# Optimization experiments

Hardware: AMD Instinct MI355X
Metric: run time of the kernel (lower is better)

Reference implementation:

```python
import jax, jax.numpy as jnp
import numpy as np

B, H, W, CP, CI = 2, 256, 256, 256, 256
IN, OUT = CP + CI, CP          # in_dims=512, out_dims=256
WS, NH, L = 8, 8, 2            # window, heads, num blocks
N = WS * WS                    # tokens per window
HD = OUT // NH                 # head dim = 32
SCALE = HD ** -0.5

def _rel_pos_index():
    c = np.stack(np.meshgrid(np.arange(WS), np.arange(WS), indexing='ij')).reshape(2, -1)
    r = (c[:, :, None] - c[:, None, :]).transpose(1, 2, 0)
    r[..., 0] += WS - 1
    r[..., 1] += WS - 1
    r[..., 0] *= 2 * WS - 1
    return r.sum(-1)  # [N, N] int

REL_IDX = _rel_pos_index()

def _attn_mask(shift):
    img = np.zeros((H, W))
    cnt = 0
    for hs in (slice(0, -WS), slice(-WS, -shift), slice(-shift, None)):
        for ws_ in (slice(0, -WS), slice(-WS, -shift), slice(-shift, None)):
            img[hs, ws_] = cnt
            cnt += 1
    m = img.reshape(H // WS, WS, W // WS, WS).transpose(0, 2, 1, 3).reshape(-1, N)
    d = m[:, None, :] - m[:, :, None]
    return jnp.asarray(np.where(d != 0, -100.0, 0.0).astype(np.float32))  # [nW, N, N]

MASK = _attn_mask(WS // 2)

def _ln(x, g, b, eps=1e-5):
    m = x.mean(-1, keepdims=True)
    v = ((x - m) ** 2).mean(-1, keepdims=True)
    return (x - m) * jax.lax.rsqrt(v + eps) * g + b

def _win_attn(x, qkv_w, qkv_b, rpb_t, proj_w, proj_b, shift):
    # x: [B,H,W,C]
    if shift > 0:
        x = jnp.roll(x, (-shift, -shift), axis=(1, 2))
    nW = (H // WS) * (W // WS)
    xw = x.reshape(B, H // WS, WS, W // WS, WS, OUT).transpose(0, 1, 3, 2, 4, 5).reshape(B, nW, N, OUT)
    qkv = (xw @ qkv_w.T + qkv_b).reshape(B, nW, N, 3, NH, HD)
    q, k, v = qkv[..., 0, :, :], qkv[..., 1, :, :], qkv[..., 2, :, :]  # [B,nW,N,NH,HD]
    attn = jnp.einsum('bwqhd,bwkhd->bwhqk', q * SCALE, k)  # [B,nW,NH,N,N]
    bias = rpb_t[REL_IDX.reshape(-1)].reshape(N, N, NH).transpose(2, 0, 1)  # [NH,N,N]
    attn = attn + bias
    if shift > 0:
        attn = attn + MASK[None, :, None, :, :]
    attn = jax.nn.softmax(attn, axis=-1)
    out = jnp.einsum('bwhqk,bwkhd->bwqhd', attn, v).reshape(B, nW, N, OUT)
    out = out @ proj_w.T + proj_b
    out = out.reshape(B, H // WS, W // WS, WS, WS, OUT).transpose(0, 1, 3, 2, 4, 5).reshape(B, H, W, OUT)
    if shift > 0:
        out = jnp.roll(out, (shift, shift), axis=(1, 2))
    return out

def setup_inputs() -> dict:
    key = jax.random.key(0)
    ks = jax.random.split(key, 12)
    s = 0.02
    p = {}
    p['pcd'] = jax.random.normal(ks[0], (B, H, W, CP), jnp.float32)
    p['img'] = jax.random.normal(ks[1], (B, H, W, CI), jnp.float32)
    p['rd_w1'] = jax.random.normal(ks[2], (4 * IN, IN), jnp.float32) * s
    p['rd_b1'] = jnp.zeros((4 * IN,), jnp.float32)
    p['rd_lng'] = jnp.ones((4 * IN,), jnp.float32)
    p['rd_lnb'] = jnp.zeros((4 * IN,), jnp.float32)
    p['rd_w2'] = jax.random.normal(ks[3], (OUT, 4 * IN), jnp.float32) * s
    p['rd_b2'] = jnp.zeros((OUT,), jnp.float32)
    p['n1g'] = jnp.ones((L, OUT), jnp.float32)
    p['n1b'] = jnp.zeros((L, OUT), jnp.float32)
    p['qkv_w'] = jax.random.normal(ks[4], (L, 3 * OUT, OUT), jnp.float32) * s
    p['qkv_b'] = jnp.zeros((L, 3 * OUT), jnp.float32)
    p['rpb'] = jax.random.normal(ks[5], (L, (2 * WS - 1) ** 2, NH), jnp.float32) * s
    p['proj_w'] = jax.random.normal(ks[6], (L, OUT, OUT), jnp.float32) * s
    p['proj_b'] = jnp.zeros((L, OUT), jnp.float32)
    p['n2g'] = jnp.ones((L, OUT), jnp.float32)
    p['n2b'] = jnp.zeros((L, OUT), jnp.float32)
    p['mlp_w1'] = jax.random.normal(ks[7], (L, 4 * OUT, OUT), jnp.float32) * s
    p['mlp_b1'] = jnp.zeros((L, 4 * OUT), jnp.float32)
    p['mlp_w2'] = jax.random.normal(ks[8], (L, OUT, 4 * OUT), jnp.float32) * s
    p['mlp_b2'] = jnp.zeros((L, OUT), jnp.float32)
    return p

def reference(pcd, img, rd_w1, rd_b1, rd_lng, rd_lnb, rd_w2, rd_b2,
              n1g, n1b, qkv_w, qkv_b, rpb, proj_w, proj_b,
              n2g, n2b, mlp_w1, mlp_b1, mlp_w2, mlp_b2):
    # reduce_dim: Linear -> LeakyReLU(0.01) -> LayerNorm -> Linear
    x = jnp.concatenate([pcd, img], axis=3)
    x = x @ rd_w1.T + rd_b1
    x = jnp.where(x > 0, x, 0.01 * x)
    x = _ln(x, rd_lng, rd_lnb)
    x = x @ rd_w2.T + rd_b2
    # two SwinTransformerBlocks (shift 0, then WS//2)
    for i in range(L):
        shift = 0 if i % 2 == 0 else WS // 2
        x = x + _win_attn(_ln(x, n1g[i], n1b[i]), qkv_w[i], qkv_b[i], rpb[i], proj_w[i], proj_b[i], shift)
        h = _ln(x, n2g[i], n2b[i])
        h = jax.nn.gelu(h @ mlp_w1[i].T + mlp_b1[i], approximate=False)
        x = x + h @ mlp_w2[i].T + mlp_b2[i]
    return x + pcd
```

## Files before the change

kernel.cpp:

```cpp
#include <hip/hip_runtime.h>
#include <math.h>

typedef __attribute__((ext_vector_type(4))) float f32x4v;
typedef __attribute__((ext_vector_type(8))) __bf16 bf16x8v;
typedef __attribute__((ext_vector_type(2))) uint u32x2v;
typedef __attribute__((ext_vector_type(4))) uint u32x4v;

#define SCALE 0.17677669529663687f
#define TOK 131072
#define MCHUNK 32768
#define T32 ((long)TOK * 32)
#define C32 ((long)MCHUNK * 32)

__device__ __forceinline__ ushort f2bf(float v){
  uint x = __float_as_uint(v);
  return (ushort)((x + 0x7fffu + ((x >> 16) & 1u)) >> 16);
}
__device__ __forceinline__ float bflo(uint u){ return __uint_as_float(u << 16); }
__device__ __forceinline__ float bfhi(uint u){ return __uint_as_float(u & 0xffff0000u); }
__device__ __forceinline__ float bf2f(ushort u){ return __uint_as_float((uint)u << 16); }

__device__ __forceinline__ void gload16(const void* g, void* l){
  __builtin_amdgcn_global_load_lds(
      (const __attribute__((address_space(1))) uint*)g,
      (__attribute__((address_space(3))) uint*)l, 16, 0, 0);
}

__global__ __launch_bounds__(256) void cvtw_k(const float* __restrict__ src,
    ushort* __restrict__ dst, int K, long m32, int n4){
  const int i = blockIdx.x * 256 + threadIdx.x;
  if (i >= n4) return;
  const int flat = i * 4;
  const int r = flat / K, k = flat % K;
  float4 v = ((const float4*)src)[i];
  ushort4 o = { f2bf(v.x), f2bf(v.y), f2bf(v.z), f2bf(v.w) };
  *(ushort4*)(dst + (long)(k >> 5) * m32 + (long)r * 32 + (k & 31)) = o;
}

__global__ __launch_bounds__(64) void cvtwg_k(const float* __restrict__ src,
    const float* __restrict__ gma, const float* __restrict__ bta,
    ushort* __restrict__ dst, float* __restrict__ c1, float* __restrict__ c2,
    int K, long m32){
  const int n = blockIdx.x, lane = threadIdx.x;
  const float* sp = src + (long)n * K;
  float s1 = 0.f, s2 = 0.f;
  for (int k = lane * 4; k < K; k += 256){
    float4 wv = *(const float4*)(sp + k);
    float4 gv = *(const float4*)(gma + k);
    float4 bv = *(const float4*)(bta + k);
    s1 += wv.x * gv.x + wv.y * gv.y + wv.z * gv.z + wv.w * gv.w;
    s2 += wv.x * bv.x + wv.y * bv.y + wv.z * bv.z + wv.w * bv.w;
    ushort4 o = { f2bf(wv.x * gv.x), f2bf(wv.y * gv.y), f2bf(wv.z * gv.z), f2bf(wv.w * gv.w) };
    *(ushort4*)(dst + (long)(k >> 5) * m32 + (long)n * 32 + (k & 31)) = o;
  }
  #pragma unroll
  for (int o = 1; o < 64; o <<= 1){ s1 += __shfl_xor(s1, o); s2 += __shfl_xor(s2, o); }
  if (lane == 0){ c1[n] = s1; c2[n] = s2; }
}

__global__ __launch_bounds__(256) void concat_k(const float* __restrict__ pcd,
    const float* __restrict__ img, ushort* __restrict__ A0){
  const long gid = (long)blockIdx.x * 256 + threadIdx.x;
  const long t = gid >> 7;
  const int c4 = (int)(gid & 127) * 4;
  const float* src = (c4 < 256) ? (pcd + t * 256 + c4) : (img + t * 256 + (c4 - 256));
  float4 v = *(const float4*)src;
  ushort4 o = { f2bf(v.x), f2bf(v.y), f2bf(v.z), f2bf(v.w) };
  const long chunk = t >> 15, tc = t & 32767;
  ushort* dst = A0 + chunk * 16777216 + (long)(c4 >> 5) * C32 + tc * 32 + (c4 & 31);
  __builtin_nontemporal_store(*(u32x2v*)&o, (u32x2v*)dst);
}

__global__ __launch_bounds__(256) void rowstats_k(const ushort* __restrict__ X,
    float* __restrict__ stats){
  const int row = blockIdx.x, tid = threadIdx.x;
  uint4 u = *(const uint4*)(X + (long)(tid >> 2) * C32 + (long)row * 32 + (tid & 3) * 8);
  float s = 0.f, q = 0.f;
  uint* e = (uint*)&u;
  #pragma unroll
  for (int c = 0; c < 4; ++c){
    float a = bflo(e[c]), b2 = bfhi(e[c]);
    s += a + b2; q += a * a + b2 * b2;
  }
  #pragma unroll
  for (int o = 1; o < 64; o <<= 1){ s += __shfl_xor(s, o); q += __shfl_xor(q, o); }
  __shared__ float ss[4], qs[4];
  if ((tid & 63) == 0){ ss[tid >> 6] = s; qs[tid >> 6] = q; }
  __syncthreads();
  if (tid == 0){
    float S = ss[0] + ss[1] + ss[2] + ss[3];
    float Q = qs[0] + qs[1] + qs[2] + qs[3];
    float mean = S * (1.f / 2048.f);
    float var = Q * (1.f / 2048.f) - mean * mean;
    stats[row * 2] = mean;
    stats[row * 2 + 1] = rsqrtf(var + 1e-5f);
  }
}

__global__ __launch_bounds__(256) void stats256b_k(const ushort* __restrict__ xb,
    float* __restrict__ stats){
  const int lane = threadIdx.x & 63, wd = threadIdx.x >> 6;
  const long row = (long)blockIdx.x * 4 + wd;
  uint2 u = *(const uint2*)(xb + (long)(lane >> 3) * T32 + row * 32 + (lane & 7) * 4);
  float a = bflo(u.x), b2 = bfhi(u.x), c = bflo(u.y), d = bfhi(u.y);
  float s = a + b2 + c + d;
  float q = a * a + b2 * b2 + c * c + d * d;
  #pragma unroll
  for (int o = 1; o < 64; o <<= 1){ s += __shfl_xor(s, o); q += __shfl_xor(q, o); }
  if (lane == 0){
    float mean = s * (1.f / 256.f);
    float var = q * (1.f / 256.f) - mean * mean;
    stats[row * 2] = mean;
    stats[row * 2 + 1] = rsqrtf(var + 1e-5f);
  }
}

template<int ACT, int OUTT, int RES, bool LNEPI, int MINB>
__global__ __launch_bounds__(256, MINB) void gemm_k(
    const ushort* __restrict__ A, const ushort* __restrict__ W,
    const float* __restrict__ bias,
    float* __restrict__ outf, ushort* __restrict__ outb,
    const ushort* __restrict__ res, const float* __restrict__ pcdp,
    const float* __restrict__ stats, const float* __restrict__ c1v,
    const float* __restrict__ c2v, int N, int K, int gx,
    long aM32, long wM32, long oM32, int mOff)
{
  __shared__ ushort As[2][128 * 32];
  __shared__ ushort Bs[2][128 * 32];
  const int tid = threadIdx.x;
  const int lane = tid & 63, w = tid >> 6;
  const int nwg = gridDim.x;
  const int xcd = blockIdx.x & 7;
  const int idx = blockIdx.x >> 3;
  const int mPerX = nwg / (8 * gx);
  const int sg = idx / (8 * gx);
  const int u  = idx - sg * (8 * gx);
  const int nT = u >> 3;
  const int ml = u & 7;
  const int mBase = (xcd * mPerX + sg * 8 + ml) * 128;
  const int nBase = nT * 128;
  const int fr = lane & 15, grp = lane >> 4;
  const int wr = w >> 1, wc = w & 1;

  f32x4v acc[4][4];
  #pragma unroll
  for (int i = 0; i < 4; ++i)
    #pragma unroll
    for (int j = 0; j < 4; ++j) acc[i][j] = (f32x4v){0.f, 0.f, 0.f, 0.f};

  const long aBase = (long)(mBase + w * 32) * 32 + lane * 8;
  const long wBase = (long)(nBase + w * 32) * 32 + lane * 8;
  const int woff = w * 1024;

  gload16(A + aBase, &As[0][woff]);
  gload16(A + aBase + 512, &As[0][woff + 512]);
  gload16(W + wBase, &Bs[0][woff]);
  gload16(W + wBase + 512, &Bs[0][woff + 512]);
  __syncthreads();

  const int NT = K >> 5;
  int cur = 0;
  for (int t = 0; t < NT; ++t){
    if (t + 1 < NT){
      const long ao = aBase + (long)(t + 1) * aM32;
      const long wo = wBase + (long)(t + 1) * wM32;
      const int nxt = cur ^ 1;
      gload16(A + ao, &As[nxt][woff]);
      gload16(A + ao + 512, &As[nxt][woff + 512]);
      gload16(W + wo, &Bs[nxt][woff]);
      gload16(W + wo + 512, &Bs[nxt][woff + 512]);
    }
    bf16x8v af[4], bv[4];
    #pragma unroll
    for (int i = 0; i < 4; ++i)
      af[i] = *(const bf16x8v*)&As[cur][(wr * 64 + i * 16 + fr) * 32 + grp * 8];
    #pragma unroll
    for (int j = 0; j < 4; ++j)
      bv[j] = *(const bf16x8v*)&Bs[cur][(wc * 64 + j * 16 + fr) * 32 + grp * 8];
    #pragma unroll
    for (int i = 0; i < 4; ++i)
      #pragma unroll
      for (int j = 0; j < 4; ++j)
        acc[i][j] = __builtin_amdgcn_mfma_f32_16x16x32_bf16(af[i], bv[j], acc[i][j], 0, 0, 0);
    __syncthreads();
    cur ^= 1;
  }

  float muv[16], rsv[16];
  if (LNEPI){
    #pragma unroll
    for (int i = 0; i < 4; ++i)
      #pragma unroll
      for (int rr = 0; rr < 4; ++rr){
        const int m = mBase + wr * 64 + i * 16 + grp * 4 + rr;
        muv[i * 4 + rr] = stats[m * 2];
        rsv[i * 4 + rr] = stats[m * 2 + 1];
      }
  }
  #pragma unroll
  for (int j = 0; j < 4; ++j){
    const int n = nBase + wc * 64 + j * 16 + fr;
    const float bn = bias[n];
    float c1n = 0.f, c2n = 0.f;
    if (LNEPI){ c1n = c1v[n]; c2n = c2v[n]; }
    #pragma unroll
    for (int i = 0; i < 4; ++i){
      #pragma unroll
      for (int rr = 0; rr < 4; ++rr){
        const long m = mBase + wr * 64 + i * 16 + grp * 4 + rr;
        float v = acc[i][j][rr];
        if (LNEPI) v = rsv[i * 4 + rr] * v - muv[i * 4 + rr] * rsv[i * 4 + rr] * c1n + c2n;
        v += bn;
        if (ACT == 1) v = v > 0.f ? v : 0.01f * v;
        if (ACT == 2){
          const float u2 = v * (0.7978845608f + 0.0356774081f * v * v);
          const float t2 = 1.f - 2.f / (__expf(2.f * u2) + 1.f);
          v = 0.5f * v * (1.f + t2);
        }
        if (RES >= 1)
          v += bf2f(res[(long)(n >> 5) * T32 + (mOff + m) * 32 + (n & 31)]);
        if (RES == 2) v += pcdp[(mOff + m) * N + n];
        acc[i][j][rr] = v;
        if (OUTT == 0) __builtin_nontemporal_store(v, &outf[(mOff + m) * N + n]);
      }
    }
  }
  if (OUTT == 1){
    ushort* eb = &As[0][0];
    __syncthreads();
    #pragma unroll
    for (int p = 0; p < 2; ++p){
      if (wr == p){
        #pragma unroll
        for (int i = 0; i < 4; ++i)
          #pragma unroll
          for (int rr = 0; rr < 4; ++rr){
            const int rl = i * 16 + grp * 4 + rr;
            #pragma unroll
            for (int j = 0; j < 4; ++j)
              eb[rl * 128 + wc * 64 + j * 16 + fr] = f2bf(acc[i][j][rr]);
          }
      }
      __syncthreads();
      #pragma unroll
      for (int it = 0; it < 4; ++it){
        const int c = it * 256 + tid;
        const int row = c >> 4, cg = c & 15;
        const u32x4v val = *(const u32x4v*)&eb[row * 128 + cg * 8];
        ushort* dst = outb + (long)((nBase >> 5) + (cg >> 2)) * oM32
                    + (long)(mOff + mBase + p * 64 + row) * 32 + (cg & 3) * 8;
        __builtin_nontemporal_store(val, (u32x4v*)dst);
      }
      __syncthreads();
    }
  }
}

template<int SHIFT>
__global__ __launch_bounds__(256, 2) void attn_k(const ushort* __restrict__ qkv,
    const float* __restrict__ rpb, ushort* __restrict__ outp)
{
  __shared__ ushort Vt[4][2312];
  __shared__ ushort Pl[4][4616];
  __shared__ float bias_s[4][226];
  __shared__ int code_s[64];
  const int tid = threadIdx.x;
  const int lane = tid & 63, wid = tid >> 6;
  const int hg = blockIdx.x & 1;
  const int bw = blockIdx.x >> 1;
  const int b = bw >> 10, widx = bw & 1023;
  const int wh = widx >> 5, ww = widx & 31;
  const int head = hg * 4 + wid;
  const int fr = lane & 15, grp = lane >> 4;

  for (int i = lane; i < 225; i += 64) bias_s[wid][i] = rpb[i * 8 + head];
  if (SHIFT > 0 && tid < 64){
    const int hh = wh * 8 + (tid >> 3), wwp = ww * 8 + (tid & 7);
    const int rh = (hh < 248) ? 0 : ((hh < 256 - SHIFT) ? 1 : 2);
    const int rw = (wwp < 248) ? 0 : ((wwp < 256 - SHIFT) ? 1 : 2);
    code_s[tid] = rh * 3 + rw;
  }
  #pragma unroll
  for (int it = 0; it < 4; ++it){
    const int c = it * 256 + tid;
    const int row = c >> 4, part = c & 15;
    const int hc = part >> 2, dc = part & 3;
    const int hs = (wh * 8 + (row >> 3) + SHIFT) & 255;
    const int wsm = (ww * 8 + (row & 7) + SHIFT) & 255;
    const long tk = ((long)b * 256 + hs) * 256 + wsm;
    const uint4 vu = *(const uint4*)(qkv + (long)(16 + hg * 4 + hc) * T32 + tk * 32 + dc * 8);
    const ushort* ve = (const ushort*)&vu;
    #pragma unroll
    for (int e = 0; e < 8; ++e)
      Vt[hc][(dc * 8 + e) * 72 + row] = ve[e];
  }
  long tokr[4];
  #pragma unroll
  for (int j = 0; j < 4; ++j){
    const int n = j * 16 + fr;
    const int hs = (wh * 8 + (n >> 3) + SHIFT) & 255;
    const int wsm = (ww * 8 + (n & 7) + SHIFT) & 255;
    tokr[j] = ((long)b * 256 + hs) * 256 + wsm;
  }
  bf16x8v kf[4];
  #pragma unroll
  for (int j = 0; j < 4; ++j)
    kf[j] = *(const bf16x8v*)(qkv + (long)(8 + head) * T32 + tokr[j] * 32 + grp * 8);
  __syncthreads();

  float invs[4][4];
  #pragma unroll
  for (int qi = 0; qi < 4; ++qi){
    const bf16x8v qf = *(const bf16x8v*)(qkv + (long)head * T32 + tokr[qi] * 32 + grp * 8);
    f32x4v sc[4];
    #pragma unroll
    for (int ci = 0; ci < 4; ++ci)
      sc[ci] = __builtin_amdgcn_mfma_f32_16x16x32_bf16(qf, kf[ci],
          (f32x4v){0.f, 0.f, 0.f, 0.f}, 0, 0, 0);
    #pragma unroll
    for (int rr = 0; rr < 4; ++rr){
      const int q = qi * 16 + grp * 4 + rr;
      const int thq = q >> 3, twq = q & 7;
      int codeq = 0;
      if (SHIFT > 0){
        const int hq = wh * 8 + thq, wq = ww * 8 + twq;
        const int rh = (hq < 248) ? 0 : ((hq < 256 - SHIFT) ? 1 : 2);
        const int rw = (wq < 248) ? 0 : ((wq < 256 - SHIFT) ? 1 : 2);
        codeq = rh * 3 + rw;
      }
      const int lbase = (thq + 7 - (fr >> 3)) * 15 + (twq + 7 - (fr & 7));
      float sum = 0.f;
      #pragma unroll
      for (int ci = 0; ci < 4; ++ci){
        float s = sc[ci][rr] * SCALE + bias_s[wid][lbase - ci * 30];
        if (SHIFT > 0 && codeq != code_s[ci * 16 + fr]) s -= 100.f;
        const float p = __expf(s);
        sum += p;
        Pl[wid][q * 72 + ci * 16 + fr] = f2bf(p);
      }
      sum += __shfl_xor(sum, 1);
      sum += __shfl_xor(sum, 2);
      sum += __shfl_xor(sum, 4);
      sum += __shfl_xor(sum, 8);
      invs[qi][rr] = 1.f / sum;
    }
  }
  f32x4v o[4][2];
  #pragma unroll
  for (int qi = 0; qi < 4; ++qi)
    #pragma unroll
    for (int di = 0; di < 2; ++di) o[qi][di] = (f32x4v){0.f, 0.f, 0.f, 0.f};
  #pragma unroll
  for (int ks = 0; ks < 2; ++ks){
    bf16x8v pa[4], bvv[2];
    #pragma unroll
    for (int qi = 0; qi < 4; ++qi)
      pa[qi] = *(const bf16x8v*)&Pl[wid][(qi * 16 + fr) * 72 + ks * 32 + grp * 8];
    #pragma unroll
    for (int di = 0; di < 2; ++di)
      bvv[di] = *(const bf16x8v*)&Vt[wid][(di * 16 + fr) * 72 + ks * 32 + grp * 8];
    #pragma unroll
    for (int qi = 0; qi < 4; ++qi)
      #pragma unroll
      for (int di = 0; di < 2; ++di)
        o[qi][di] = __builtin_amdgcn_mfma_f32_16x16x32_bf16(pa[qi], bvv[di], o[qi][di], 0, 0, 0);
  }
  #pragma unroll
  for (int qi = 0; qi < 4; ++qi)
    #pragma unroll
    for (int di = 0; di < 2; ++di)
      #pragma unroll
      for (int rr = 0; rr < 4; ++rr)
        Pl[wid][(qi * 16 + grp * 4 + rr) * 72 + di * 16 + fr] =
            f2bf(o[qi][di][rr] * invs[qi][rr]);
  {
    const int n = lane;
    const int hs = (wh * 8 + (n >> 3) + SHIFT) & 255;
    const int wsm = (ww * 8 + (n & 7) + SHIFT) & 255;
    const long tokL = ((long)b * 256 + hs) * 256 + wsm;
    ushort* ob = outp + (long)head * T32 + tokL * 32;
    #pragma unroll
    for (int c4 = 0; c4 < 4; ++c4)
      *(uint4*)(ob + c4 * 8) = *(const uint4*)&Pl[wid][n * 72 + c4 * 8];
  }
}

extern "C" void kernel_launch(void* const* d_in, const int* in_sizes, int n_in,
                              void* d_out, int out_size, void* d_ws, size_t ws_size,
                              hipStream_t stream){
  const float* pcd    = (const float*)d_in[0];
  const float* img    = (const float*)d_in[1];
  const float* rd_w1  = (const float*)d_in[2];
  const float* rd_b1  = (const float*)d_in[3];
  const float* rd_lng = (const float*)d_in[4];
  const float* rd_lnb = (const float*)d_in[5];
  const float* rd_w2  = (const float*)d_in[6];
  const float* rd_b2  = (const float*)d_in[7];
  const float* n1g    = (const float*)d_in[8];
  const float* n1b    = (const float*)d_in[9];
  const float* qkv_w  = (const float*)d_in[10];
  const float* qkv_b  = (const float*)d_in[11];
  const float* rpb    = (const float*)d_in[12];
  const float* proj_w = (const float*)d_in[13];
  const float* proj_b = (const float*)d_in[14];
  const float* n2g    = (const float*)d_in[15];
  const float* n2b    = (const float*)d_in[16];
  const float* mlp_w1 = (const float*)d_in[17];
  const float* mlp_b1 = (const float*)d_in[18];
  const float* mlp_w2 = (const float*)d_in[19];
  const float* mlp_b2 = (const float*)d_in[20];

  char* ws = (char*)d_ws;
  ushort* w1b    = (ushort*)(ws + 0);
  ushort* w2g    = (ushort*)(ws + 2097152);
  ushort* qkvwg  = (ushort*)(ws + 3145728);
  ushort* projwb = (ushort*)(ws + 3932160);
  ushort* mlp1wg = (ushort*)(ws + 4194304);
  ushort* mlp2wb = (ushort*)(ws + 5242880);
  float*  cvec   = (float*)(ws + 6291456);
  float*  w2c1   = cvec,        *w2c2   = cvec + 256;
  float*  qkvc1  = cvec + 512,  *qkvc2  = cvec + 2048;
  float*  mlp1c1 = cvec + 3584, *mlp1c2 = cvec + 5632;
  float*  stats  = (float*)(ws + 6324224);
  ushort* xr     = (ushort*)(ws + 7372800);
  char*   big    = ws + 74481664;
  ushort* A0     = (ushort*)big;
  ushort* X1c    = (ushort*)(big + 134217728);
  ushort* qkvb   = (ushort*)big;
  ushort* attno  = (ushort*)(big + 201326592);
  ushort* hidden = (ushort*)big;
  float* xout = (float*)d_out;

  cvtw_k<<<1024, 256, 0, stream>>>(rd_w1, w1b, 512, 65536, 262144);
  cvtwg_k<<<256, 64, 0, stream>>>(rd_w2, rd_lng, rd_lnb, w2g, w2c1, w2c2, 2048, 8192);
  for (int i = 0; i < 2; ++i){
    cvtw_k<<<64,  256, 0, stream>>>(proj_w + i * 65536, projwb + i * 65536, 256, 8192, 16384);
    cvtw_k<<<256, 256, 0, stream>>>(mlp_w2 + i * 262144, mlp2wb + i * 262144, 1024, 8192, 65536);
    cvtwg_k<<<768, 64, 0, stream>>>(qkv_w + i * 196608, n1g + i * 256, n1b + i * 256,
        qkvwg + i * 196608, qkvc1 + i * 768, qkvc2 + i * 768, 256, 24576);
    cvtwg_k<<<1024, 64, 0, stream>>>(mlp_w1 + i * 262144, n2g + i * 256, n2b + i * 256,
        mlp1wg + i * 262144, mlp1c1 + i * 1024, mlp1c2 + i * 1024, 256, 32768);
  }
  concat_k<<<65536, 256, 0, stream>>>(pcd, img, A0);

  for (int c = 0; c < 4; ++c){
    const long off = (long)c * MCHUNK;
    gemm_k<1,1,0,false,2><<<4096, 256, 0, stream>>>(A0 + (long)c * 16777216, w1b, rd_b1,
        nullptr, X1c, nullptr, nullptr, nullptr, nullptr, nullptr,
        2048, 512, 16, C32, 65536, C32, 0);
    rowstats_k<<<MCHUNK, 256, 0, stream>>>(X1c, stats + off * 2);
    gemm_k<0,1,0,true,2><<<512, 256, 0, stream>>>(X1c, w2g, rd_b2,
        nullptr, xr, nullptr, nullptr,
        stats + off * 2, w2c1, w2c2,
        256, 2048, 2, C32, 8192, T32, (int)off);
  }
  stats256b_k<<<TOK / 4, 256, 0, stream>>>(xr, stats);

  for (int i = 0; i < 2; ++i){
    gemm_k<0,1,0,true,2><<<6144, 256, 0, stream>>>(xr, qkvwg + i * 196608, qkv_b + i * 768,
        nullptr, qkvb, nullptr, nullptr, stats, qkvc1 + i * 768, qkvc2 + i * 768,
        768, 256, 6, T32, 24576, T32, 0);
    if (i == 0)
      attn_k<0><<<4096, 256, 0, stream>>>(qkvb, rpb, attno);
    else
      attn_k<4><<<4096, 256, 0, stream>>>(qkvb, rpb + 1800, attno);
    gemm_k<0,1,1,false,2><<<2048, 256, 0, stream>>>(attno, projwb + i * 65536,
        proj_b + i * 256, nullptr, xr, xr, nullptr, nullptr, nullptr, nullptr,
        256, 256, 2, T32, 8192, T32, 0);
    stats256b_k<<<TOK / 4, 256, 0, stream>>>(xr, stats);
    gemm_k<2,1,0,true,2><<<8192, 256, 0, stream>>>(xr, mlp1wg + i * 262144,
        mlp_b1 + i * 1024, nullptr, hidden, nullptr, nullptr,
        stats, mlp1c1 + i * 1024, mlp1c2 + i * 1024,
        1024, 256, 8, T32, 32768, T32, 0);
    if (i == 0){
      gemm_k<0,1,1,false,2><<<2048, 256, 0, stream>>>(hidden, mlp2wb, mlp_b2,
          nullptr, xr, xr, nullptr, nullptr, nullptr, nullptr,
          256, 1024, 2, T32, 8192, T32, 0);
      stats256b_k<<<TOK / 4, 256, 0, stream>>>(xr, stats);
    } else {
      gemm_k<0,0,2,false,2><<<2048, 256, 0, stream>>>(hidden, mlp2wb + 262144,
          mlp_b2 + 256, xout, nullptr, xr, pcd, nullptr, nullptr, nullptr,
          256, 1024, 2, T32, 8192, T32, 0);
    }
  }
}
```

Measured before the change: 1.998 ms.

## Replace LDS-direct double buffering with register-staged prefetch and single LDS buffer

The GEMM kernel no longer uses global_load_lds into two LDS buffers. It prefetches the next K-tile into registers, writes it to a single LDS buffer after the MFMAs, and then issues the loads for the tile after that. LDS use per block is halved, which could raise occupancy. In exchange the loop needs two barriers per iteration and extra VGPRs, and global latency is hidden only behind one compute step.

```diff
diff --git a/kernel.cpp b/kernel.cpp
--- a/kernel.cpp
+++ b/kernel.cpp
@@ -19,12 +19,6 @@
 __device__ __forceinline__ float bflo(uint u){ return __uint_as_float(u << 16); }
 __device__ __forceinline__ float bfhi(uint u){ return __uint_as_float(u & 0xffff0000u); }
 __device__ __forceinline__ float bf2f(ushort u){ return __uint_as_float((uint)u << 16); }
-
-__device__ __forceinline__ void gload16(const void* g, void* l){
-  __builtin_amdgcn_global_load_lds(
-      (const __attribute__((address_space(1))) uint*)g,
-      (__attribute__((address_space(3))) uint*)l, 16, 0, 0);
-}
 
 __global__ __launch_bounds__(256) void cvtw_k(const float* __restrict__ src,
     ushort* __restrict__ dst, int K, long m32, int n4){
@@ -125,8 +119,7 @@
     const float* __restrict__ c2v, int N, int K, int gx,
     long aM32, long wM32, long oM32, int mOff)
 {
-  __shared__ ushort As[2][128 * 32];
-  __shared__ ushort Bs[2][128 * 32];
+  __shared__ ushort SH[8192];
   const int tid = threadIdx.x;
   const int lane = tid & 63, w = tid >> 6;
   const int nwg = gridDim.x;
@@ -150,40 +143,51 @@
 
   const long aBase = (long)(mBase + w * 32) * 32 + lane * 8;
   const long wBase = (long)(nBase + w * 32) * 32 + lane * 8;
-  const int woff = w * 1024;
-
-  gload16(A + aBase, &As[0][woff]);
-  gload16(A + aBase + 512, &As[0][woff + 512]);
-  gload16(W + wBase, &Bs[0][woff]);
-  gload16(W + wBase + 512, &Bs[0][woff + 512]);
+  ushort* Ad = &SH[w * 1024 + lane * 8];
+  ushort* Bd = &SH[4096 + w * 1024 + lane * 8];
+
+  const int NT = K >> 5;
+  uint4 a0 = *(const uint4*)(A + aBase);
+  uint4 a1 = *(const uint4*)(A + aBase + 512);
+  uint4 b0 = *(const uint4*)(W + wBase);
+  uint4 b1 = *(const uint4*)(W + wBase + 512);
+  *(uint4*)Ad = a0; *(uint4*)(Ad + 512) = a1;
+  *(uint4*)Bd = b0; *(uint4*)(Bd + 512) = b1;
+  if (NT > 1){
+    a0 = *(const uint4*)(A + aBase + aM32);
+    a1 = *(const uint4*)(A + aBase + aM32 + 512);
+    b0 = *(const uint4*)(W + wBase + wM32);
+    b1 = *(const uint4*)(W + wBase + wM32 + 512);
+  }
   __syncthreads();
 
-  const int NT = K >> 5;
-  int cur = 0;
   for (int t = 0; t < NT; ++t){
-    if (t + 1 < NT){
-      const long ao = aBase + (long)(t + 1) * aM32;
-      const long wo = wBase + (long)(t + 1) * wM32;
-      const int nxt = cur ^ 1;
-      gload16(A + ao, &As[nxt][woff]);
-      gload16(A + ao + 512, &As[nxt][woff + 512]);
-      gload16(W + wo, &Bs[nxt][woff]);
-      gload16(W + wo + 512, &Bs[nxt][woff + 512]);
-    }
     bf16x8v af[4], bv[4];
     #pragma unroll
     for (int i = 0; i < 4; ++i)
-      af[i] = *(const bf16x8v*)&As[cur][(wr * 64 + i * 16 + fr) * 32 + grp * 8];
+      af[i] = *(const bf16x8v*)&SH[(wr * 64 + i * 16 + fr) * 32 + grp * 8];
     #pragma unroll
     for (int j = 0; j < 4; ++j)
-      bv[j] = *(const bf16x8v*)&Bs[cur][(wc * 64 + j * 16 + fr) * 32 + grp * 8];
+      bv[j] = *(const bf16x8v*)&SH[4096 + (wc * 64 + j * 16 + fr) * 32 + grp * 8];
     #pragma unroll
     for (int i = 0; i < 4; ++i)
       #pragma unroll
       for (int j = 0; j < 4; ++j)
         acc[i][j] = __builtin_amdgcn_mfma_f32_16x16x32_bf16(af[i], bv[j], acc[i][j], 0, 0, 0);
-    __syncthreads();
-    cur ^= 1;
+    if (t + 1 < NT){
+      __syncthreads();
+      *(uint4*)Ad = a0; *(uint4*)(Ad + 512) = a1;
+      *(uint4*)Bd = b0; *(uint4*)(Bd + 512) = b1;
+      if (t + 2 < NT){
+        const long ao = aBase + (long)(t + 2) * aM32;
+        const long wo = wBase + (long)(t + 2) * wM32;
+        a0 = *(const uint4*)(A + ao);
+        a1 = *(const uint4*)(A + ao + 512);
+        b0 = *(const uint4*)(W + wo);
+        b1 = *(const uint4*)(W + wo + 512);
+      }
+      __syncthreads();
+    }
   }
 
   float muv[16], rsv[16];
@@ -226,7 +230,7 @@
     }
   }
   if (OUTT == 1){
-    ushort* eb = &As[0][0];
+    ushort* eb = &SH[0];
     __syncthreads();
     #pragma unroll
     for (int p = 0; p < 2; ++p){
```

New measurement: 1.880 ms. 1.06x faster.
